# Kernel tuning notes

Hardware: AMD Instinct MI355X
Metric: run time of the kernel (lower is better)

## Reference

```python
import jax, jax.numpy as jnp
import numpy as np

N, F, H, C, E, L = 100000, 512, 64, 40, 1600000, 6


def setup_inputs() -> dict:
    key = jax.random.key(0)
    ks = jax.random.split(key, 2 * L + 4)
    x = jax.random.normal(ks[0], (N, F), dtype=jnp.float32)
    edge_index = jax.random.randint(ks[1], (2, E), 0, N, dtype=jnp.int32)
    inp = {"x": x, "edge_index": edge_index}
    in_dims = [F + H * i for i in range(L)]  # 512, 576, ..., 832 (dense concat)
    for i in range(L):
        inp[f"W{i}"] = jax.random.normal(ks[2 + i], (in_dims[i], H), dtype=jnp.float32) / np.sqrt(in_dims[i]).astype(np.float32)
        inp[f"b{i}"] = jnp.zeros((H,), dtype=jnp.float32)
    jk_dim = in_dims[-1] + H  # 896 = num_features + 6*H
    inp["Wlin"] = jax.random.normal(ks[2 + L], (jk_dim, C), dtype=jnp.float32) / np.sqrt(jk_dim).astype(np.float32)
    inp["blin"] = jnp.zeros((C,), dtype=jnp.float32)
    return inp


def _gcn_norm(edge_index, num_nodes, dtype):
    # Add self loops, compute symmetric normalization deg^-1/2 * deg^-1/2
    loop = jnp.arange(num_nodes, dtype=edge_index.dtype)
    row = jnp.concatenate([edge_index[0], loop])  # source
    col = jnp.concatenate([edge_index[1], loop])  # target
    deg = jax.ops.segment_sum(jnp.ones_like(col, dtype=dtype), col, num_segments=num_nodes)
    dinv = jnp.where(deg > 0, jax.lax.rsqrt(jnp.maximum(deg, 1.0)), 0.0)
    norm = dinv[row] * dinv[col]  # [E + N]
    return row, col, norm


def reference(x, edge_index, W0, b0, W1, b1, W2, b2, W3, b3, W4, b4, W5, b5, Wlin, blin):
    Ws = [W0, W1, W2, W3, W4, W5]
    bs = [b0, b1, b2, b3, b4, b5]
    n = x.shape[0]
    row, col, norm = _gcn_norm(edge_index, n, x.dtype)

    xs = [x]
    for W, b in zip(Ws, bs):
        inp = jnp.concatenate(xs, axis=1)          # dense (DenseNet-style) concat
        lin = inp @ W                               # [n, H] transform before propagate
        msg = lin[row] * norm[:, None]              # gather + edge weight
        agg = jax.ops.segment_sum(msg, col, num_segments=n)  # scatter-add aggregate
        h = jax.nn.relu(agg + b)                    # GCNConv bias, then ReLU (dropout = eval mode)
        xs.append(h)

    hcat = jnp.concatenate(xs, axis=1)              # JumpingKnowledge('cat')
    logits = hcat @ Wlin + blin
    return jax.nn.log_softmax(logits, axis=1)
```

## Files before the change

kernel.cpp:

```cpp
#include <hip/hip_runtime.h>
#include <hip/hip_bf16.h>

#define HH 64
#define XDIM 896
#define FF 512
#define LL 6
#define CC 40
#define CBSZ 512
#define SLACK 10240

typedef __bf16 bf16x8 __attribute__((ext_vector_type(8)));
typedef float f32x4 __attribute__((ext_vector_type(4)));

__device__ __forceinline__ unsigned short f2bf(float f){
  union{float f; unsigned int u;} v; v.f=f; unsigned int u=v.u;
  return (unsigned short)((u + 0x7fffu + ((u>>16)&1u))>>16);
}
__device__ __forceinline__ float u2f(unsigned u){
  union{unsigned u; float f;} v; v.u=u; return v.f;
}

__global__ void __launch_bounds__(256) k_xcast(const float* __restrict__ x, unsigned short* __restrict__ X,
                                               unsigned short* __restrict__ lin, int* __restrict__ bcur,
                                               int N, int NB){
  int i = blockIdx.x*blockDim.x + threadIdx.x;
  if (i < 32) ((unsigned*)(lin + (size_t)N*64))[i] = 0u;
  if (i < NB) bcur[i] = i*SLACK;
  int total = N*(FF/4);
  if (i >= total) return;
  int row = i/(FF/4), c4 = (i%(FF/4))*4;
  float4 v = *(const float4*)(x + (size_t)row*FF + c4);
  ushort4 o; o.x=f2bf(v.x); o.y=f2bf(v.y); o.z=f2bf(v.z); o.w=f2bf(v.w);
  *(ushort4*)(X + (size_t)row*XDIM + c4) = o;
}

struct WfA {
  const float* W[7];
  unsigned short* dst[7];
  int nt[7], nc[7];
  int off[8];
};
__global__ void __launch_bounds__(256) k_wfrag(WfA A){
  int idx = blockIdx.x*256 + threadIdx.x;
  if (idx >= A.off[7]) return;
  int seg = 0;
  while (idx >= A.off[seg+1]) ++seg;
  int li = idx - A.off[seg];
  int j = li&7, lane=(li>>3)&63, rem=li>>9;
  int ntile = A.nt[seg], ncols = A.nc[seg];
  int nt = rem % ntile, kb = rem / ntile;
  int k = kb*32 + (lane>>4)*8 + j;
  int c = nt*16 + (lane&15);
  float v = (c<ncols)? A.W[seg][(size_t)k*ncols + c] : 0.f;
  A.dst[seg][li]=f2bf(v);
}

__global__ void __launch_bounds__(256) k_part(const int* __restrict__ ei, int E, int CH, int NB,
                                              int* __restrict__ bcur, unsigned* __restrict__ tmp){
  __shared__ int hist[256];
  __shared__ int run[256];
  int t=threadIdx.x, b=blockIdx.x;
  int lo=b*CH, hi=lo+CH; if (hi>E) hi=E;
  for (int i=t;i<NB;i+=256) hist[i]=0;
  __syncthreads();
  for (int i=lo+t;i<hi;i+=256) atomicAdd(&hist[ei[E+i]>>9], 1);
  __syncthreads();
  for (int i=t;i<NB;i+=256) run[i]=atomicAdd(&bcur[i], hist[i]);
  __syncthreads();
  for (int i=lo+t;i<hi;i+=256){
    int r=ei[i], c=ei[E+i];
    int pos=atomicAdd(&run[c>>9],1);
    tmp[pos]=((unsigned)r<<9)|(unsigned)(c&(CBSZ-1));
  }
}

__global__ void __launch_bounds__(1024) k_build(const unsigned* __restrict__ tmp,
                                                const int* __restrict__ bcur,
                                                int* __restrict__ offsS, int* __restrict__ offsE,
                                                float* __restrict__ dinv,
                                                int* __restrict__ esrc, int N){
  __shared__ int cnt[CBSZ];
  __shared__ int run[CBSZ];
  int t=threadIdx.x, b=blockIdx.x;
  int n0=b*CBSZ;
  int nloc=N-n0; if (nloc>CBSZ) nloc=CBSZ;
  int wbase=b*SLACK;
  int wend=bcur[b];
  if (t<CBSZ) cnt[t]=0;
  __syncthreads();
  for (int i=wbase+t; i<wend; i+=1024) atomicAdd(&cnt[tmp[i]&(CBSZ-1u)],1);
  __syncthreads();
  int v = (t<CBSZ)? cnt[t] : 0;
  if (t<CBSZ) run[t]=v;
  __syncthreads();
  for (int o=1;o<CBSZ;o<<=1){
    int xx = (t<CBSZ && t>=o)? run[t-o] : 0;
    __syncthreads();
    if (t<CBSZ) run[t]+=xx;
    __syncthreads();
  }
  if (t<nloc){
    int s = wbase + (run[t]-v);
    offsS[n0+t]=s;
    offsE[n0+t]=s+v;
    dinv[n0+t]=rsqrtf((float)(v+1));
    run[t]=s;
  }
  __syncthreads();
  for (int i=wbase+t; i<wend; i+=1024){
    unsigned vv=tmp[i];
    int pos=atomicAdd(&run[vv&(CBSZ-1u)],1);
    esrc[pos]=(int)(vv>>9);
  }
}

__global__ void __launch_bounds__(256) k_gemm(const unsigned short* __restrict__ X,
                                              const unsigned short* __restrict__ Wf,
                                              const float* __restrict__ dinv,
                                              unsigned short* __restrict__ lin,
                                              int N, int nkb){
  int lane = threadIdx.x & 63, wid = threadIdx.x >> 6;
  long row0 = (long)blockIdx.x*128 + wid*32;
  int arow = lane & 15, kgrp = lane >> 4;
  long r0 = row0 + arow;      if (r0 > (long)N-1) r0 = N-1;
  long r1 = row0 + 16 + arow; if (r1 > (long)N-1) r1 = N-1;
  const unsigned short* ap0 = X + (size_t)r0*XDIM + kgrp*8;
  const unsigned short* ap1 = X + (size_t)r1*XDIM + kgrp*8;
  const unsigned short* bptr = Wf + lane*8;
  f32x4 acc00={0.f,0.f,0.f,0.f}, acc01=acc00, acc02=acc00, acc03=acc00;
  f32x4 acc10=acc00, acc11=acc00, acc12=acc00, acc13=acc00;
  for (int kb=0; kb<nkb; ++kb){
    bf16x8 a0 = *(const bf16x8*)(ap0 + (size_t)kb*32);
    bf16x8 a1 = *(const bf16x8*)(ap1 + (size_t)kb*32);
    const unsigned short* bp = bptr + (size_t)kb*2048;
    bf16x8 b0=*(const bf16x8*)bp, b1=*(const bf16x8*)(bp+512),
           b2=*(const bf16x8*)(bp+1024), b3=*(const bf16x8*)(bp+1536);
    acc00=__builtin_amdgcn_mfma_f32_16x16x32_bf16(a0,b0,acc00,0,0,0);
    acc10=__builtin_amdgcn_mfma_f32_16x16x32_bf16(a1,b0,acc10,0,0,0);
    acc01=__builtin_amdgcn_mfma_f32_16x16x32_bf16(a0,b1,acc01,0,0,0);
    acc11=__builtin_amdgcn_mfma_f32_16x16x32_bf16(a1,b1,acc11,0,0,0);
    acc02=__builtin_amdgcn_mfma_f32_16x16x32_bf16(a0,b2,acc02,0,0,0);
    acc12=__builtin_amdgcn_mfma_f32_16x16x32_bf16(a1,b2,acc12,0,0,0);
    acc03=__builtin_amdgcn_mfma_f32_16x16x32_bf16(a0,b3,acc03,0,0,0);
    acc13=__builtin_amdgcn_mfma_f32_16x16x32_bf16(a1,b3,acc13,0,0,0);
  }
  for (int j=0;j<4;++j){
    long rr = row0 + kgrp*4 + j;
    if (rr < N){
      float dv = dinv[rr];
      unsigned short* lp = lin + (size_t)rr*64 + arow;
      lp[0]  = f2bf(acc00[j]*dv);
      lp[16] = f2bf(acc01[j]*dv);
      lp[32] = f2bf(acc02[j]*dv);
      lp[48] = f2bf(acc03[j]*dv);
    }
    long rr1 = rr + 16;
    if (rr1 < N){
      float dv = dinv[rr1];
      unsigned short* lp = lin + (size_t)rr1*64 + arow;
      lp[0]  = f2bf(acc10[j]*dv);
      lp[16] = f2bf(acc11[j]*dv);
      lp[32] = f2bf(acc12[j]*dv);
      lp[48] = f2bf(acc13[j]*dv);
    }
  }
}

__global__ void __launch_bounds__(256) k_agg(const unsigned short* __restrict__ lin,
                                             const int* __restrict__ offsS,
                                             const int* __restrict__ offsE,
                                             const int* __restrict__ esrc,
                                             const float* __restrict__ dinv,
                                             const float* __restrict__ bias,
                                             unsigned short* __restrict__ X,
                                             int colbase, int N){
  int lane = threadIdx.x & 63, wid = threadIdx.x >> 6;
  int n = blockIdx.x*4 + wid;
  if (n >= N) return;
  int sub = lane >> 4;
  int fq  = lane & 15;
  const unsigned short* lq = lin + fq*4;
  float a0=0.f, a1=0.f, a2=0.f, a3=0.f;
  int s = offsS[n], e = offsE[n];
  int base = s;
  for (; base + 32 <= e; base += 32){
    #pragma unroll
    for (int k=0;k<8;++k){
      int sx = esrc[base + 4*k + sub];
      uint2 v = *(const uint2*)(lq + (size_t)sx*64);
      a0 += u2f(v.x<<16); a1 += u2f(v.x&0xffff0000u);
      a2 += u2f(v.y<<16); a3 += u2f(v.y&0xffff0000u);
    }
  }
  if (base < e){
    int rem = e - base;
    if (rem > 16){
      #pragma unroll
      for (int k=0;k<8;++k){
        int idx = 4*k + sub;
        int sx = esrc[base + idx];
        sx = (idx < rem) ? sx : (int)N;
        uint2 v = *(const uint2*)(lq + (size_t)sx*64);
        a0 += u2f(v.x<<16); a1 += u2f(v.x&0xffff0000u);
        a2 += u2f(v.y<<16); a3 += u2f(v.y&0xffff0000u);
      }
    } else {
      #pragma unroll
      for (int k=0;k<4;++k){
        int idx = 4*k + sub;
        int sx = esrc[base + idx];
        sx = (idx < rem) ? sx : (int)N;
        uint2 v = *(const uint2*)(lq + (size_t)sx*64);
        a0 += u2f(v.x<<16); a1 += u2f(v.x&0xffff0000u);
        a2 += u2f(v.y<<16); a3 += u2f(v.y&0xffff0000u);
      }
    }
  }
  a0 += __shfl_xor(a0,16,64); a0 += __shfl_xor(a0,32,64);
  a1 += __shfl_xor(a1,16,64); a1 += __shfl_xor(a1,32,64);
  a2 += __shfl_xor(a2,16,64); a2 += __shfl_xor(a2,32,64);
  a3 += __shfl_xor(a3,16,64); a3 += __shfl_xor(a3,32,64);
  uint2 vs = *(const uint2*)(lq + (size_t)n*64);
  a0 += u2f(vs.x<<16); a1 += u2f(vs.x&0xffff0000u);
  a2 += u2f(vs.y<<16); a3 += u2f(vs.y&0xffff0000u);
  float dv = dinv[n];
  float4 b4 = *(const float4*)(bias + fq*4);
  float h0 = fmaxf(a0*dv + b4.x, 0.f);
  float h1 = fmaxf(a1*dv + b4.y, 0.f);
  float h2 = fmaxf(a2*dv + b4.z, 0.f);
  float h3 = fmaxf(a3*dv + b4.w, 0.f);
  if (sub == 0){
    ushort4 o; o.x=f2bf(h0); o.y=f2bf(h1); o.z=f2bf(h2); o.w=f2bf(h3);
    *(ushort4*)(X + (size_t)n*XDIM + colbase + fq*4) = o;
  }
}

__global__ void __launch_bounds__(256) k_final(const unsigned short* __restrict__ X,
                                               const unsigned short* __restrict__ Wf,
                                               const float* __restrict__ blin,
                                               float* __restrict__ out, int N){
  int lane=threadIdx.x&63, wid=threadIdx.x>>6;
  long row0=(long)blockIdx.x*64 + wid*16;
  int c0=lane&15, g=lane>>4;
  long r=row0+c0; if (r > (long)N-1) r = N-1;
  const unsigned short* aptr = X + (size_t)r*XDIM + g*8;
  const unsigned short* bptr = Wf + lane*8;
  f32x4 acc0={0.f,0.f,0.f,0.f}, acc1=acc0, acc2=acc0;
  const int nkb = XDIM/32;
  for (int kb=0;kb<nkb;++kb){
    bf16x8 a=*(const bf16x8*)(aptr+(size_t)kb*32);
    const unsigned short* bp = bptr + (size_t)kb*1536;
    bf16x8 b0=*(const bf16x8*)bp, b1=*(const bf16x8*)(bp+512), b2=*(const bf16x8*)(bp+1024);
    acc0=__builtin_amdgcn_mfma_f32_16x16x32_bf16(a,b0,acc0,0,0,0);
    acc1=__builtin_amdgcn_mfma_f32_16x16x32_bf16(a,b1,acc1,0,0,0);
    acc2=__builtin_amdgcn_mfma_f32_16x16x32_bf16(a,b2,acc2,0,0,0);
  }
  float bl0 = blin[c0], bl1 = blin[16+c0];
  bool v2ok = (c0 < 8);
  float bl2 = v2ok ? blin[32+c0] : 0.f;
  for (int j=0;j<4;++j){
    long rr = row0 + g*4 + j;
    float v0 = acc0[j]+bl0, v1 = acc1[j]+bl1;
    float v2 = v2ok ? (acc2[j]+bl2) : -1e30f;
    float m = fmaxf(fmaxf(v0,v1),v2);
    m = fmaxf(m, __shfl_xor(m,1,64));
    m = fmaxf(m, __shfl_xor(m,2,64));
    m = fmaxf(m, __shfl_xor(m,4,64));
    m = fmaxf(m, __shfl_xor(m,8,64));
    float sEx = expf(v0-m)+expf(v1-m)+(v2ok?expf(v2-m):0.f);
    sEx += __shfl_xor(sEx,1,64);
    sEx += __shfl_xor(sEx,2,64);
    sEx += __shfl_xor(sEx,4,64);
    sEx += __shfl_xor(sEx,8,64);
    float lse = m + logf(sEx);
    if (rr < N){
      out[(size_t)rr*CC + c0]      = v0 - lse;
      out[(size_t)rr*CC + 16 + c0] = v1 - lse;
      if (v2ok) out[(size_t)rr*CC + 32 + c0] = v2 - lse;
    }
  }
}

extern "C" void kernel_launch(void* const* d_in, const int* in_sizes, int n_in,
                              void* d_out, int out_size, void* d_ws, size_t ws_size,
                              hipStream_t stream){
  const float* x = (const float*)d_in[0];
  const int* ei = (const int*)d_in[1];
  const float* Wl[LL]; const float* bl[LL];
  for (int i=0;i<LL;i++){ Wl[i]=(const float*)d_in[2+2*i]; bl[i]=(const float*)d_in[3+2*i]; }
  const float* Wlin = (const float*)d_in[2+2*LL];
  const float* blin = (const float*)d_in[3+2*LL];
  float* out = (float*)d_out;
  const int N = in_sizes[0]/FF;
  const int E = in_sizes[1]/2;
  const int NB = (N+CBSZ-1)/CBSZ;

  char* p = (char*)d_ws;
  auto alloc = [&](size_t bb)->char*{ char* r=p; p += (bb+255)&~(size_t)255; return r; };
  unsigned short* X   = (unsigned short*)alloc((size_t)N*XDIM*2);
  unsigned short* lin = (unsigned short*)alloc((size_t)(N+1)*64*2);
  unsigned* tmp = (unsigned*)lin;
  unsigned short* WfL[LL+1];
  for (int i=0;i<LL;i++){ int d=FF+HH*i; WfL[i]=(unsigned short*)alloc((size_t)d*64*2); }
  WfL[LL] = (unsigned short*)alloc((size_t)XDIM*48*2);
  float* dinv  = (float*)alloc((size_t)N*4);
  int* offsS   = (int*)alloc((size_t)N*4);
  int* offsE   = (int*)alloc((size_t)N*4);
  int* bcur    = (int*)alloc((size_t)NB*4);
  int* esrc    = (int*)alloc((size_t)NB*SLACK*4);

  k_xcast<<<(N*(FF/4)+255)/256, 256, 0, stream>>>(x, X, lin, bcur, N, NB);

  WfA A;
  int off = 0;
  for (int i=0;i<LL;i++){
    A.W[i]=Wl[i]; A.dst[i]=WfL[i]; A.nt[i]=4; A.nc[i]=HH;
    A.off[i]=off; off += ((FF+HH*i)>>5)*4*512;
  }
  A.W[LL]=Wlin; A.dst[LL]=WfL[LL]; A.nt[LL]=3; A.nc[LL]=CC;
  A.off[LL]=off; off += (XDIM>>5)*3*512;
  A.off[LL+1]=off;
  k_wfrag<<<(off+255)/256, 256, 0, stream>>>(A);

  int CH = (E+255)/256;
  k_part <<<256, 256, 0, stream>>>(ei, E, CH, NB, bcur, tmp);
  k_build<<<NB, 1024, 0, stream>>>(tmp, bcur, offsS, offsE, dinv, esrc, N);

  int gb = (N+127)/128;
  int ab = (N+3)/4;
  for (int i=0;i<LL;i++){
    k_gemm<<<gb,256,0,stream>>>(X, WfL[i], dinv, lin, N, (FF+HH*i)>>5);
    k_agg <<<ab,256,0,stream>>>(lin, offsS, offsE, esrc, dinv, bl[i], X, FF+HH*i, N);
  }
  k_final<<<(N+63)/64,256,0,stream>>>(X, WfL[LL], blin, out, N);
}
```

Baseline: 608.9 us.

## Precompute x-part of all layer GEMMs in one batched GEMM and merge prep kernels

All six layer weights and the final linear weight are packed into one large fragment matrix for the shared 512-wide x block. A single k_gbig kernel multiplies x by it once, storing per-layer partial products in bf16 and the classifier partial in fp32. Each layer GEMM and the final GEMM then only process the newly concatenated hidden columns and add the stored partial, so the input features are no longer re-read six times. The prep kernels (cast, weight fragmenting, edge partition) are fused into one launch, and bcur is now zeroed with a memset. In exchange the code needs extra workspace for five partial buffers, and rounding the partials to bf16 adds precision loss.

```diff
diff --git a/kernel.cpp b/kernel.cpp
--- a/kernel.cpp
+++ b/kernel.cpp
@@ -8,6 +8,7 @@
 #define CC 40
 #define CBSZ 512
 #define SLACK 10240
+#define NSEG 13
 
 typedef __bf16 bf16x8 __attribute__((ext_vector_type(8)));
 typedef float f32x4 __attribute__((ext_vector_type(4)));
@@ -16,61 +17,66 @@
   union{float f; unsigned int u;} v; v.f=f; unsigned int u=v.u;
   return (unsigned short)((u + 0x7fffu + ((u>>16)&1u))>>16);
 }
+__device__ __forceinline__ float bf2f(unsigned short u){
+  union{unsigned int u; float f;} v; v.u = ((unsigned int)u)<<16; return v.f;
+}
 __device__ __forceinline__ float u2f(unsigned u){
   union{unsigned u; float f;} v; v.u=u; return v.f;
 }
 
-__global__ void __launch_bounds__(256) k_xcast(const float* __restrict__ x, unsigned short* __restrict__ X,
-                                               unsigned short* __restrict__ lin, int* __restrict__ bcur,
-                                               int N, int NB){
-  int i = blockIdx.x*blockDim.x + threadIdx.x;
-  if (i < 32) ((unsigned*)(lin + (size_t)N*64))[i] = 0u;
-  if (i < NB) bcur[i] = i*SLACK;
-  int total = N*(FF/4);
-  if (i >= total) return;
-  int row = i/(FF/4), c4 = (i%(FF/4))*4;
-  float4 v = *(const float4*)(x + (size_t)row*FF + c4);
-  ushort4 o; o.x=f2bf(v.x); o.y=f2bf(v.y); o.z=f2bf(v.z); o.w=f2bf(v.w);
-  *(ushort4*)(X + (size_t)row*XDIM + c4) = o;
-}
-
-struct WfA {
-  const float* W[7];
-  unsigned short* dst[7];
-  int nt[7], nc[7];
-  int off[8];
+struct PrepP {
+  const float* x; const int* ei;
+  unsigned short* X; unsigned short* lin;
+  int* bcur; unsigned* tmp;
+  const float* W[NSEG]; unsigned short* dst[NSEG];
+  int nt[NSEG], nc[NSEG], tst[NSEG], tbs[NSEG], kbase[NSEG];
+  int off[NSEG+1];
+  int N, E, CH, NB, WB;
 };
-__global__ void __launch_bounds__(256) k_wfrag(WfA A){
-  int idx = blockIdx.x*256 + threadIdx.x;
-  if (idx >= A.off[7]) return;
-  int seg = 0;
-  while (idx >= A.off[seg+1]) ++seg;
-  int li = idx - A.off[seg];
-  int j = li&7, lane=(li>>3)&63, rem=li>>9;
-  int ntile = A.nt[seg], ncols = A.nc[seg];
-  int nt = rem % ntile, kb = rem / ntile;
-  int k = kb*32 + (lane>>4)*8 + j;
-  int c = nt*16 + (lane&15);
-  float v = (c<ncols)? A.W[seg][(size_t)k*ncols + c] : 0.f;
-  A.dst[seg][li]=f2bf(v);
-}
-
-__global__ void __launch_bounds__(256) k_part(const int* __restrict__ ei, int E, int CH, int NB,
-                                              int* __restrict__ bcur, unsigned* __restrict__ tmp){
+
+__global__ void __launch_bounds__(256) k_prep(PrepP P){
   __shared__ int hist[256];
   __shared__ int run[256];
   int t=threadIdx.x, b=blockIdx.x;
-  int lo=b*CH, hi=lo+CH; if (hi>E) hi=E;
-  for (int i=t;i<NB;i+=256) hist[i]=0;
-  __syncthreads();
-  for (int i=lo+t;i<hi;i+=256) atomicAdd(&hist[ei[E+i]>>9], 1);
-  __syncthreads();
-  for (int i=t;i<NB;i+=256) run[i]=atomicAdd(&bcur[i], hist[i]);
-  __syncthreads();
-  for (int i=lo+t;i<hi;i+=256){
-    int r=ei[i], c=ei[E+i];
-    int pos=atomicAdd(&run[c>>9],1);
-    tmp[pos]=((unsigned)r<<9)|(unsigned)(c&(CBSZ-1));
+  if (b < 256){
+    int E=P.E;
+    int lo=b*P.CH, hi=lo+P.CH; if (hi>E) hi=E;
+    for (int i=t;i<P.NB;i+=256) hist[i]=0;
+    __syncthreads();
+    for (int i=lo+t;i<hi;i+=256) atomicAdd(&hist[P.ei[E+i]>>9], 1);
+    __syncthreads();
+    for (int i=t;i<P.NB;i+=256) run[i]=i*SLACK+atomicAdd(&P.bcur[i], hist[i]);
+    __syncthreads();
+    for (int i=lo+t;i<hi;i+=256){
+      int r=P.ei[i], c=P.ei[E+i];
+      int pos=atomicAdd(&run[c>>9],1);
+      P.tmp[pos]=((unsigned)r<<9)|(unsigned)(c&(CBSZ-1));
+    }
+  } else if (b < 256+P.WB){
+    int idx=(b-256)*256+t;
+    if (idx < P.off[NSEG]){
+      int seg=0;
+      while (idx>=P.off[seg+1]) ++seg;
+      int li=idx-P.off[seg];
+      int j=li&7, ln=(li>>3)&63, rem2=li>>9;
+      int ntile=P.nt[seg], ncols=P.nc[seg];
+      int nt_=rem2%ntile, kb=rem2/ntile;
+      int k=P.kbase[seg]+kb*32+(ln>>4)*8+j;
+      int c=nt_*16+(ln&15);
+      float v=(c<ncols)? P.W[seg][(size_t)k*ncols+c] : 0.f;
+      int di = ((kb*P.tst[seg] + P.tbs[seg] + nt_)*64 + ln)*8 + j;
+      P.dst[seg][di]=f2bf(v);
+    }
+  } else {
+    int i=(b-256-P.WB)*256+t;
+    if (i<32) ((unsigned*)(P.lin+(size_t)P.N*64))[i]=0u;
+    int total=P.N*(FF/4);
+    if (i<total){
+      int row=i/(FF/4), c4=(i%(FF/4))*4;
+      float4 v=*(const float4*)(P.x+(size_t)row*FF+c4);
+      ushort4 o; o.x=f2bf(v.x); o.y=f2bf(v.y); o.z=f2bf(v.z); o.w=f2bf(v.w);
+      *(ushort4*)(P.X+(size_t)row*XDIM+c4)=o;
+    }
   }
 }
 
@@ -85,7 +91,7 @@
   int n0=b*CBSZ;
   int nloc=N-n0; if (nloc>CBSZ) nloc=CBSZ;
   int wbase=b*SLACK;
-  int wend=bcur[b];
+  int wend=wbase + bcur[b];
   if (t<CBSZ) cnt[t]=0;
   __syncthreads();
   for (int i=wbase+t; i<wend; i+=1024) atomicAdd(&cnt[tmp[i]&(CBSZ-1u)],1);
@@ -114,22 +120,84 @@
   }
 }
 
-__global__ void __launch_bounds__(256) k_gemm(const unsigned short* __restrict__ X,
-                                              const unsigned short* __restrict__ Wf,
-                                              const float* __restrict__ dinv,
-                                              unsigned short* __restrict__ lin,
-                                              int N, int nkb){
+struct GBP {
+  const unsigned short* X; const unsigned short* WfBig;
+  const float* dinv;
+  unsigned short* pl[6];
+  float* pF;
+  int N;
+};
+
+__global__ void __launch_bounds__(256) k_gbig(GBP P){
+  int t=threadIdx.x, lane=t&63, wid=t>>6;
+  int wpair=wid>>1, whalf=wid&1;
+  int tb = whalf ? 13 : 0;
+  long row0 = (long)blockIdx.x*64 + wpair*32;
+  int arow=lane&15, kgrp=lane>>4;
+  long r0=row0+arow;    if (r0>(long)P.N-1) r0=P.N-1;
+  long r1=row0+16+arow; if (r1>(long)P.N-1) r1=P.N-1;
+  const unsigned short* ap0 = P.X + (size_t)r0*XDIM + kgrp*8;
+  const unsigned short* ap1 = P.X + (size_t)r1*XDIM + kgrp*8;
+  const unsigned short* bbase = P.WfBig + (size_t)tb*512 + lane*8;
+  f32x4 acc0[14], acc1[14];
+  #pragma unroll
+  for (int i=0;i<14;i++){ f32x4 z={0.f,0.f,0.f,0.f}; acc0[i]=z; acc1[i]=z; }
+  for (int kb=0;kb<16;++kb){
+    bf16x8 a0=*(const bf16x8*)(ap0+(size_t)kb*32);
+    bf16x8 a1=*(const bf16x8*)(ap1+(size_t)kb*32);
+    const unsigned short* bp = bbase + (size_t)kb*27*512;
+    #pragma unroll
+    for (int tt=0;tt<14;++tt){
+      bf16x8 b=*(const bf16x8*)(bp + tt*512);
+      acc0[tt]=__builtin_amdgcn_mfma_f32_16x16x32_bf16(a0,b,acc0[tt],0,0,0);
+      acc1[tt]=__builtin_amdgcn_mfma_f32_16x16x32_bf16(a1,b,acc1[tt],0,0,0);
+    }
+  }
+  #pragma unroll
+  for (int tt=0;tt<14;++tt){
+    int tg = tb+tt;
+    if (whalf && tt==0) continue;
+    #pragma unroll
+    for (int j=0;j<4;++j){
+      long rr=row0+kgrp*4+j, rr1=rr+16;
+      if (tg<24){
+        int li=tg>>2, tloc=tg&3;
+        if (rr<P.N){
+          float s = (li==0) ? P.dinv[rr] : 1.f;
+          P.pl[li][(size_t)rr*64 + tloc*16 + arow] = f2bf(acc0[tt][j]*s);
+        }
+        if (rr1<P.N){
+          float s = (li==0) ? P.dinv[rr1] : 1.f;
+          P.pl[li][(size_t)rr1*64 + tloc*16 + arow] = f2bf(acc1[tt][j]*s);
+        }
+      } else {
+        int c=(tg-24)*16+arow;
+        if (c<CC){
+          if (rr<P.N)  P.pF[(size_t)rr*CC+c]=acc0[tt][j];
+          if (rr1<P.N) P.pF[(size_t)rr1*CC+c]=acc1[tt][j];
+        }
+      }
+    }
+  }
+}
+
+__global__ void __launch_bounds__(256) k_gemmH(const unsigned short* __restrict__ X,
+                                               const unsigned short* __restrict__ WfH,
+                                               const unsigned short* __restrict__ part,
+                                               const float* __restrict__ dinv,
+                                               unsigned short* __restrict__ lin,
+                                               int N, int nkb2){
   int lane = threadIdx.x & 63, wid = threadIdx.x >> 6;
   long row0 = (long)blockIdx.x*128 + wid*32;
   int arow = lane & 15, kgrp = lane >> 4;
   long r0 = row0 + arow;      if (r0 > (long)N-1) r0 = N-1;
   long r1 = row0 + 16 + arow; if (r1 > (long)N-1) r1 = N-1;
-  const unsigned short* ap0 = X + (size_t)r0*XDIM + kgrp*8;
-  const unsigned short* ap1 = X + (size_t)r1*XDIM + kgrp*8;
-  const unsigned short* bptr = Wf + lane*8;
+  const unsigned short* ap0 = X + (size_t)r0*XDIM + FF + kgrp*8;
+  const unsigned short* ap1 = X + (size_t)r1*XDIM + FF + kgrp*8;
+  const unsigned short* bptr = WfH + lane*8;
   f32x4 acc00={0.f,0.f,0.f,0.f}, acc01=acc00, acc02=acc00, acc03=acc00;
   f32x4 acc10=acc00, acc11=acc00, acc12=acc00, acc13=acc00;
-  for (int kb=0; kb<nkb; ++kb){
+  for (int kb=0; kb<nkb2; ++kb){
     bf16x8 a0 = *(const bf16x8*)(ap0 + (size_t)kb*32);
     bf16x8 a1 = *(const bf16x8*)(ap1 + (size_t)kb*32);
     const unsigned short* bp = bptr + (size_t)kb*2048;
@@ -148,20 +216,22 @@
     long rr = row0 + kgrp*4 + j;
     if (rr < N){
       float dv = dinv[rr];
+      const unsigned short* pp = part + (size_t)rr*64 + arow;
       unsigned short* lp = lin + (size_t)rr*64 + arow;
-      lp[0]  = f2bf(acc00[j]*dv);
-      lp[16] = f2bf(acc01[j]*dv);
-      lp[32] = f2bf(acc02[j]*dv);
-      lp[48] = f2bf(acc03[j]*dv);
+      lp[0]  = f2bf((acc00[j]+bf2f(pp[0]))*dv);
+      lp[16] = f2bf((acc01[j]+bf2f(pp[16]))*dv);
+      lp[32] = f2bf((acc02[j]+bf2f(pp[32]))*dv);
+      lp[48] = f2bf((acc03[j]+bf2f(pp[48]))*dv);
     }
     long rr1 = rr + 16;
     if (rr1 < N){
       float dv = dinv[rr1];
+      const unsigned short* pp = part + (size_t)rr1*64 + arow;
       unsigned short* lp = lin + (size_t)rr1*64 + arow;
-      lp[0]  = f2bf(acc10[j]*dv);
-      lp[16] = f2bf(acc11[j]*dv);
-      lp[32] = f2bf(acc12[j]*dv);
-      lp[48] = f2bf(acc13[j]*dv);
+      lp[0]  = f2bf((acc10[j]+bf2f(pp[0]))*dv);
+      lp[16] = f2bf((acc11[j]+bf2f(pp[16]))*dv);
+      lp[32] = f2bf((acc12[j]+bf2f(pp[32]))*dv);
+      lp[48] = f2bf((acc13[j]+bf2f(pp[48]))*dv);
     }
   }
 }
@@ -237,16 +307,17 @@
 
 __global__ void __launch_bounds__(256) k_final(const unsigned short* __restrict__ X,
                                                const unsigned short* __restrict__ Wf,
+                                               const float* __restrict__ pF,
                                                const float* __restrict__ blin,
                                                float* __restrict__ out, int N){
   int lane=threadIdx.x&63, wid=threadIdx.x>>6;
   long row0=(long)blockIdx.x*64 + wid*16;
   int c0=lane&15, g=lane>>4;
   long r=row0+c0; if (r > (long)N-1) r = N-1;
-  const unsigned short* aptr = X + (size_t)r*XDIM + g*8;
+  const unsigned short* aptr = X + (size_t)r*XDIM + FF + g*8;
   const unsigned short* bptr = Wf + lane*8;
   f32x4 acc0={0.f,0.f,0.f,0.f}, acc1=acc0, acc2=acc0;
-  const int nkb = XDIM/32;
+  const int nkb = (XDIM-FF)/32;
   for (int kb=0;kb<nkb;++kb){
     bf16x8 a=*(const bf16x8*)(aptr+(size_t)kb*32);
     const unsigned short* bp = bptr + (size_t)kb*1536;
@@ -260,8 +331,10 @@
   float bl2 = v2ok ? blin[32+c0] : 0.f;
   for (int j=0;j<4;++j){
     long rr = row0 + g*4 + j;
-    float v0 = acc0[j]+bl0, v1 = acc1[j]+bl1;
-    float v2 = v2ok ? (acc2[j]+bl2) : -1e30f;
+    long rrc = rr < N ? rr : (long)N-1;
+    const float* pp = pF + (size_t)rrc*CC;
+    float v0 = acc0[j]+bl0+pp[c0], v1 = acc1[j]+bl1+pp[16+c0];
+    float v2 = v2ok ? (acc2[j]+bl2+pp[32+c0]) : -1e30f;
     float m = fmaxf(fmaxf(v0,v1),v2);
     m = fmaxf(m, __shfl_xor(m,1,64));
     m = fmaxf(m, __shfl_xor(m,2,64));
@@ -300,37 +373,58 @@
   unsigned short* X   = (unsigned short*)alloc((size_t)N*XDIM*2);
   unsigned short* lin = (unsigned short*)alloc((size_t)(N+1)*64*2);
   unsigned* tmp = (unsigned*)lin;
-  unsigned short* WfL[LL+1];
-  for (int i=0;i<LL;i++){ int d=FF+HH*i; WfL[i]=(unsigned short*)alloc((size_t)d*64*2); }
-  WfL[LL] = (unsigned short*)alloc((size_t)XDIM*48*2);
+  unsigned short* WfBig  = (unsigned short*)alloc((size_t)16*27*512*2);
+  unsigned short* WfH[LL];
+  for (int i=1;i<LL;i++) WfH[i]=(unsigned short*)alloc((size_t)(2*i)*4*512*2);
+  unsigned short* WfLinH = (unsigned short*)alloc((size_t)12*3*512*2);
+  unsigned short* part[LL];
+  for (int i=1;i<LL;i++) part[i]=(unsigned short*)alloc((size_t)N*64*2);
+  float* pF    = (float*)alloc((size_t)N*CC*4);
   float* dinv  = (float*)alloc((size_t)N*4);
   int* offsS   = (int*)alloc((size_t)N*4);
   int* offsE   = (int*)alloc((size_t)N*4);
   int* bcur    = (int*)alloc((size_t)NB*4);
-  int* esrc    = (int*)alloc((size_t)NB*SLACK*4);
-
-  k_xcast<<<(N*(FF/4)+255)/256, 256, 0, stream>>>(x, X, lin, bcur, N, NB);
-
-  WfA A;
-  int off = 0;
+  int* esrc    = (int*)alloc(((size_t)NB*SLACK+64)*4);
+
+  PrepP P;
+  P.x=x; P.ei=ei; P.X=X; P.lin=lin; P.bcur=bcur; P.tmp=tmp;
+  int off=0, sg=0;
   for (int i=0;i<LL;i++){
-    A.W[i]=Wl[i]; A.dst[i]=WfL[i]; A.nt[i]=4; A.nc[i]=HH;
-    A.off[i]=off; off += ((FF+HH*i)>>5)*4*512;
-  }
-  A.W[LL]=Wlin; A.dst[LL]=WfL[LL]; A.nt[LL]=3; A.nc[LL]=CC;
-  A.off[LL]=off; off += (XDIM>>5)*3*512;
-  A.off[LL+1]=off;
-  k_wfrag<<<(off+255)/256, 256, 0, stream>>>(A);
-
-  int CH = (E+255)/256;
-  k_part <<<256, 256, 0, stream>>>(ei, E, CH, NB, bcur, tmp);
+    P.W[sg]=Wl[i]; P.dst[sg]=WfBig; P.nt[sg]=4; P.nc[sg]=HH;
+    P.tst[sg]=27; P.tbs[sg]=4*i; P.kbase[sg]=0;
+    P.off[sg]=off; off += 16*4*512; ++sg;
+  }
+  P.W[sg]=Wlin; P.dst[sg]=WfBig; P.nt[sg]=3; P.nc[sg]=CC;
+  P.tst[sg]=27; P.tbs[sg]=24; P.kbase[sg]=0;
+  P.off[sg]=off; off += 16*3*512; ++sg;
+  for (int i=1;i<LL;i++){
+    P.W[sg]=Wl[i]; P.dst[sg]=WfH[i]; P.nt[sg]=4; P.nc[sg]=HH;
+    P.tst[sg]=4; P.tbs[sg]=0; P.kbase[sg]=FF;
+    P.off[sg]=off; off += (2*i)*4*512; ++sg;
+  }
+  P.W[sg]=Wlin; P.dst[sg]=WfLinH; P.nt[sg]=3; P.nc[sg]=CC;
+  P.tst[sg]=3; P.tbs[sg]=0; P.kbase[sg]=FF;
+  P.off[sg]=off; off += 12*3*512; ++sg;
+  P.off[sg]=off;
+  P.N=N; P.E=E; P.CH=(E+255)/256; P.NB=NB; P.WB=(off+255)/256;
+  int XB=(N*(FF/4)+255)/256;
+
+  hipMemsetAsync(bcur, 0, (size_t)NB*4, stream);
+  k_prep <<<256 + P.WB + XB, 256, 0, stream>>>(P);
   k_build<<<NB, 1024, 0, stream>>>(tmp, bcur, offsS, offsE, dinv, esrc, N);
+
+  GBP G;
+  G.X=X; G.WfBig=WfBig; G.dinv=dinv;
+  G.pl[0]=lin;
+  for (int i=1;i<LL;i++) G.pl[i]=part[i];
+  G.pF=pF; G.N=N;
+  k_gbig<<<(N+63)/64, 256, 0, stream>>>(G);
 
   int gb = (N+127)/128;
   int ab = (N+3)/4;
   for (int i=0;i<LL;i++){
-    k_gemm<<<gb,256,0,stream>>>(X, WfL[i], dinv, lin, N, (FF+HH*i)>>5);
-    k_agg <<<ab,256,0,stream>>>(lin, offsS, offsE, esrc, dinv, bl[i], X, FF+HH*i, N);
-  }
-  k_final<<<(N+63)/64,256,0,stream>>>(X, WfL[LL], blin, out, N);
-}
+    if (i>0) k_gemmH<<<gb,256,0,stream>>>(X, WfH[i], part[i], dinv, lin, N, 2*i);
+    k_agg<<<ab,256,0,stream>>>(lin, offsS, offsE, esrc, dinv, bl[i], X, FF+HH*i, N);
+  }
+  k_final<<<(N+63)/64,256,0,stream>>>(X, WfLinH, pF, blin, out, N);
+}
```

New measurement: 774.8 us. 1.27x slower.
